# Kernel tuning notes

Measured on AMD Instinct MI355X. Metric: run time of the kernel, lower is better.

## Reference

```python
import jax, jax.numpy as jnp
import numpy as np

B, N, H = 8, 512, 256
D2 = H // 2          # per-direction hidden = attention proj = 128
VOCAB, EMB = 100, 256
DIN0 = EMB + 3


def _sru_pp_layer(x, pad, Wq, Wk, Wv, Wu, vf, vr, bf, br):
    # x: (L, Bt, din); pad: (L, Bt) bool, True = padded position
    L, Bt, _ = x.shape
    d2 = Wu.shape[1] // 8
    q = x @ Wq                                   # (L,Bt,proj) attention projection
    k = q @ Wk
    v = q @ Wv
    scale = 1.0 / jnp.sqrt(jnp.asarray(q.shape[-1], q.dtype))
    scores = jnp.einsum('lbp,mbp->blm', q, k) * scale
    scores = jnp.where(pad.T[:, None, :], -1e9, scores)
    a = jnp.einsum('blm,mbp->lbp', jax.nn.softmax(scores, axis=-1), v) + q
    U = (a @ Wu).reshape(L, Bt, 2, 4, d2)        # 2 directions x 4 matrices

    def run_dir(Ud, padd, vf_d, vr_d, bf_d, br_d):
        def step(c, inp):
            u, p = inp                            # u: (Bt,4,d2), p: (Bt,)
            f = jax.nn.sigmoid(u[:, 1] + vf_d * c + bf_d)
            r = jax.nn.sigmoid(u[:, 2] + vr_d * c + br_d)
            c_new = f * c + (1.0 - f) * u[:, 0]
            c_new = jnp.where(p[:, None], c, c_new)
            h = jnp.where(p[:, None], 0.0, r * c_new + (1.0 - r) * u[:, 3])
            return c_new, h
        c0 = jnp.zeros((Bt, d2), x.dtype)
        _, hs = jax.lax.scan(step, c0, (Ud, padd))
        return hs

    hf = run_dir(U[:, :, 0], pad, vf[0], vr[0], bf[0], br[0])
    hb = run_dir(U[::-1, :, 1], pad[::-1], vf[1], vr[1], bf[1], br[1])[::-1]
    return jnp.concatenate([hf, hb], axis=-1)     # (L,Bt,2*d2)


def _forward(noisy_seqs, noisy_cords, mask, emb, params):
    Bb, Nn = noisy_seqs.shape
    X = noisy_cords[:, :, 1]                      # CA coordinates (B,N,3)
    m3 = mask[..., None]
    center = (X * m3).sum(1) / m3.sum(1)
    Xc = X - center[:, None] * m3
    C = jnp.einsum('bni,bnj->bij', Xc, Xc)        # (B,3,3) covariance
    _, V = jnp.linalg.eigh(jax.lax.stop_gradient(C))
    ops = jnp.asarray([[i, j, k] for i in (-1, 1) for j in (-1, 1) for k in (-1, 1)], X.dtype)
    F_ops = ops[None, :, None, :] * V[:, None]    # (B,8,3,3) sign-flipped frames
    hX = jnp.einsum('boji,bpj->bopi', F_ops, Xc).reshape(Bb * 8, Nn, 3)
    seq = jnp.where(noisy_seqs < 0, 82, noisy_seqs)
    hS = jnp.broadcast_to(emb[seq][:, None], (Bb, 8, Nn, emb.shape[1])).reshape(Bb * 8, Nn, -1)
    h = jnp.swapaxes(jnp.concatenate([hX, hS], -1), 0, 1)   # (N, B*8, EMB+3)
    pad = jnp.broadcast_to((mask == 0.0)[:, None], (Bb, 8, Nn)).reshape(Bb * 8, Nn).T
    for p in params:
        h = _sru_pp_layer(h, pad, *p)
    return jnp.swapaxes(h, 0, 1).reshape(Bb, 8, Nn, -1).mean(1)


def setup_inputs():
    key = jax.random.key(0)
    ks = [jax.random.fold_in(key, i) for i in range(32)]
    inp = {
        'noisy_seqs': jax.random.randint(ks[0], (B, N), 0, VOCAB, dtype=jnp.int32),
        'noisy_cords': jax.random.normal(ks[1], (B, N, 4, 3), jnp.float32),
        'mask': jnp.ones((B, N), jnp.float32),
        'emb': 0.02 * jax.random.normal(ks[2], (VOCAB, EMB), jnp.float32),
    }
    i = 3
    for l, din in enumerate([DIN0, H]):
        inp[f'Wq{l}'] = jax.random.normal(ks[i], (din, D2), jnp.float32) / np.sqrt(din); i += 1
        inp[f'Wk{l}'] = jax.random.normal(ks[i], (D2, D2), jnp.float32) / np.sqrt(D2); i += 1
        inp[f'Wv{l}'] = jax.random.normal(ks[i], (D2, D2), jnp.float32) / np.sqrt(D2); i += 1
        inp[f'Wu{l}'] = jax.random.normal(ks[i], (D2, 8 * D2), jnp.float32) / np.sqrt(D2); i += 1
        inp[f'vf{l}'] = 0.1 * jax.random.normal(ks[i], (2, D2), jnp.float32); i += 1
        inp[f'vr{l}'] = 0.1 * jax.random.normal(ks[i], (2, D2), jnp.float32); i += 1
        inp[f'bf{l}'] = jnp.zeros((2, D2), jnp.float32)
        inp[f'br{l}'] = jnp.zeros((2, D2), jnp.float32)
    return inp


def reference(noisy_seqs, noisy_cords, mask, emb,
              Wq0, Wk0, Wv0, Wu0, vf0, vr0, bf0, br0,
              Wq1, Wk1, Wv1, Wu1, vf1, vr1, bf1, br1):
    params = [(Wq0, Wk0, Wv0, Wu0, vf0, vr0, bf0, br0),
              (Wq1, Wk1, Wv1, Wu1, vf1, vr1, bf1, br1)]
    return _forward(noisy_seqs, noisy_cords, mask, emb, params)
```

## Files before the change

### kernel.cpp

```cpp
#include <hip/hip_runtime.h>
#include <hip/hip_bf16.h>
#include <math.h>

#define L_    512
#define F_    64
#define M_    (F_*L_)
#define D2_   128
#define H_    256
#define LOG2E_ 1.4426950408889634f

typedef unsigned short u16;
typedef __attribute__((ext_vector_type(8))) short s16x8;
typedef __attribute__((ext_vector_type(4))) float f32x4;

__device__ inline u16 bf_hi(float x) {
  union { float f; unsigned u; } v; v.f = x;
  unsigned r = v.u + 0x7fffu + ((v.u >> 16) & 1u);
  return (u16)(r >> 16);
}
__device__ inline float bf_to_f(u16 h) {
  union { float f; unsigned u; } v; v.u = ((unsigned)h) << 16; return v.f;
}
__device__ inline void split2(float x, u16& h, u16& l) {
  h = bf_hi(x);
  l = bf_hi(x - bf_to_f(h));
}
__device__ inline float exp2_fast(float x) {
#if __has_builtin(__builtin_amdgcn_exp2f)
  return __builtin_amdgcn_exp2f(x);
#else
  return __expf(x * 0.6931471805599453f);
#endif
}
__device__ inline float rcp_fast(float x) {
#if __has_builtin(__builtin_amdgcn_rcpf)
  return __builtin_amdgcn_rcpf(x);
#else
  return 1.f/x;
#endif
}

#define RSPLIT_A 18432
#define RSPLIT_B 26624

__global__ void geom_kernel(const float* __restrict__ cords, const float* __restrict__ mask,
                            float* __restrict__ misc) {
  int b = blockIdx.x;
  int t = threadIdx.x;
  __shared__ float red[4][256];
  float sx=0.f, sy=0.f, sz=0.f, sm=0.f;
  for (int l = t; l < 512; l += 256) {
    float m = mask[b*512 + l];
    const float* X = cords + ((size_t)(b*512 + l)*4 + 1)*3;
    sx += X[0]*m; sy += X[1]*m; sz += X[2]*m; sm += m;
  }
  red[0][t]=sx; red[1][t]=sy; red[2][t]=sz; red[3][t]=sm;
  __syncthreads();
  for (int off=128; off>0; off>>=1) {
    if (t < off) { red[0][t]+=red[0][t+off]; red[1][t]+=red[1][t+off];
                   red[2][t]+=red[2][t+off]; red[3][t]+=red[3][t+off]; }
    __syncthreads();
  }
  float inv = 1.f/red[3][0];
  float cx = red[0][0]*inv, cy = red[1][0]*inv, cz = red[2][0]*inv;
  __syncthreads();
  __shared__ float red6[6][256];
  float c00=0,c01=0,c02=0,c11=0,c12=0,c22=0;
  for (int l = t; l < 512; l += 256) {
    float m = mask[b*512+l];
    const float* X = cords + ((size_t)(b*512+l)*4 + 1)*3;
    float x = X[0]-cx*m, y = X[1]-cy*m, z = X[2]-cz*m;
    c00+=x*x; c01+=x*y; c02+=x*z; c11+=y*y; c12+=y*z; c22+=z*z;
  }
  red6[0][t]=c00; red6[1][t]=c01; red6[2][t]=c02;
  red6[3][t]=c11; red6[4][t]=c12; red6[5][t]=c22;
  __syncthreads();
  for (int off=128; off>0; off>>=1) {
    if (t < off) for (int j=0;j<6;j++) red6[j][t]+=red6[j][t+off];
    __syncthreads();
  }
  if (t == 0) {
    double A[3][3], V[3][3];
    A[0][0]=red6[0][0]; A[0][1]=A[1][0]=red6[1][0]; A[0][2]=A[2][0]=red6[2][0];
    A[1][1]=red6[3][0]; A[1][2]=A[2][1]=red6[4][0]; A[2][2]=red6[5][0];
    for (int j=0;j<3;j++) for (int i=0;i<3;i++) V[j][i] = (i==j)?1.0:0.0;
    for (int sweep=0; sweep<10; ++sweep) {
      for (int p=0;p<2;p++) for (int q=p+1;q<3;q++) {
        double apq = A[p][q];
        if (fabs(apq) < 1e-18) continue;
        double app = A[p][p], aqq = A[q][q];
        double tau = (aqq - app) / (2.0*apq);
        double tt = (tau >= 0.0) ? 1.0/(tau + sqrt(1.0+tau*tau))
                                 : 1.0/(tau - sqrt(1.0+tau*tau));
        double cc = 1.0/sqrt(1.0+tt*tt), ss = tt*cc;
        A[p][p] = app - tt*apq;
        A[q][q] = aqq + tt*apq;
        A[p][q] = A[q][p] = 0.0;
        int r = 3 - p - q;
        double arp = A[r][p], arq = A[r][q];
        A[r][p] = A[p][r] = cc*arp - ss*arq;
        A[r][q] = A[q][r] = ss*arp + cc*arq;
        for (int rr2=0; rr2<3; ++rr2) {
          double vrp = V[rr2][p], vrq = V[rr2][q];
          V[rr2][p] = cc*vrp - ss*vrq;
          V[rr2][q] = ss*vrp + cc*vrq;
        }
      }
    }
    double w[3] = {A[0][0], A[1][1], A[2][2]};
    int idx[3] = {0,1,2};
    for (int i=0;i<2;i++) for (int j=0;j<2-i;j++)
      if (w[idx[j]] > w[idx[j+1]]) { int tmp=idx[j]; idx[j]=idx[j+1]; idx[j+1]=tmp; }
    for (int jj=0;jj<3;jj++) for (int ii=0;ii<3;ii++)
      misc[b*12 + jj*3 + ii] = (float)V[jj][idx[ii]];
    misc[b*12+9]=cx; misc[b*12+10]=cy; misc[b*12+11]=cz;
  }
}

__global__ void build_h0(const int* __restrict__ seqs, const float* __restrict__ cords,
                         const float* __restrict__ mask, const float* __restrict__ emb,
                         const float* __restrict__ misc,
                         u16* __restrict__ h0h, u16* __restrict__ h0l) {
  int t = threadIdx.x;
  int r = blockIdx.x*4 + (t >> 6);
  int lane = t & 63;
  int f = r >> 9, l = r & 511;
  int b = f >> 3, o = f & 7;
  u16* rh = h0h + (size_t)r * 288;
  u16* rl = h0l + (size_t)r * 288;
  if (lane == 0) {
    float m = mask[b*512 + l];
    const float* X = cords + ((size_t)(b*512 + l)*4 + 1)*3;
    const float* mb = misc + b*12;
    float x = X[0]-mb[9]*m, y = X[1]-mb[10]*m, z = X[2]-mb[11]*m;
    #pragma unroll
    for (int i=0;i<3;i++) {
      float sgn = ((o >> (2-i)) & 1) ? 1.f : -1.f;
      float val = sgn * (mb[0+i]*x + mb[3+i]*y + mb[6+i]*z);
      u16 h,lo; split2(val,h,lo); rh[i]=h; rl[i]=lo;
    }
  }
  if (lane < 29) { rh[259+lane] = 0; rl[259+lane] = 0; }
  int s = seqs[b*512 + l];
  if (s < 0) s = 82;
  const float4 e4 = *((const float4*)(emb + (size_t)s*256) + lane);
  float ev[4] = {e4.x, e4.y, e4.z, e4.w};
  #pragma unroll
  for (int i=0;i<4;i++) {
    u16 h,lo; split2(ev[i],h,lo);
    rh[3 + lane*4 + i] = h; rl[3 + lane*4 + i] = lo;
  }
}

__global__ void prep_wqkv_mul(const float* __restrict__ Wq, const float* __restrict__ Wk,
                              const float* __restrict__ Wv,
                              float* __restrict__ wqk, float* __restrict__ wqv) {
  int k = blockIdx.x;
  int y = blockIdx.y;
  int t = threadIdx.x;
  __shared__ float row[128];
  row[t] = Wq[(size_t)k*128 + t];
  __syncthreads();
  const float* W2 = y ? Wv : Wk;
  float acc = 0.f;
  for (int j = 0; j < 128; j++) acc += row[j] * W2[(size_t)j*128 + t];
  (y ? wqv : wqk)[(size_t)k*128 + t] = acc;
}

__global__ void prep_wT3(const float* __restrict__ Wq, const float* __restrict__ wqk,
                         const float* __restrict__ wqv,
                         u16* __restrict__ Th, u16* __restrict__ Tl,
                         int K, int KP) {
  int y = blockIdx.y;
  int n = blockIdx.x;
  const float* W = (y==0) ? Wq : (y==1) ? wqk : wqv;
  int row = y*128 + n;
  for (int k = threadIdx.x; k < KP; k += 128) {
    float x = (k < K) ? W[(size_t)k*128 + n] : 0.f;
    u16 h,l; split2(x,h,l);
    Th[(size_t)row*KP + k] = h; Tl[(size_t)row*KP + k] = l;
  }
}

__global__ void prep_wu(const float* __restrict__ Wu, u16* __restrict__ Th, u16* __restrict__ Tl,
                        const float* __restrict__ bfv, const float* __restrict__ brv,
                        float* __restrict__ nbf, float* __restrict__ nbr) {
  int n = blockIdx.x;
  int dir = blockIdx.y;
  int k = threadIdx.x;
  int d = n >> 2, g = n & 3;
  float x = Wu[(size_t)k*1024 + (dir*4+g)*128 + d];
  if (g == 1 || g == 2) x *= -LOG2E_;
  u16 h,l; split2(x,h,l);
  size_t o = ((size_t)dir*512 + n)*128 + k;
  Th[o]=h; Tl[o]=l;
  if (n == 0) {
    nbf[dir*128 + k] = bfv[dir*128 + k] * (-LOG2E_);
    nbr[dir*128 + k] = brv[dir*128 + k] * (-LOG2E_);
  }
}

template<int EPI>
__global__ __launch_bounds__(256) void gemm_bb(
    const u16* __restrict__ Ah, const u16* __restrict__ Al,
    const u16* __restrict__ Bh, const u16* __restrict__ Bl,
    int KP, int lda, int ldb,
    long aBatch, long bBatch, long cBatch,
    u16* __restrict__ Ch, u16* __restrict__ Cl, int ldc,
    u16* __restrict__ Dh, u16* __restrict__ Dl,
    u16* __restrict__ Eh, u16* __restrict__ El,
    float* __restrict__ F0, float* __restrict__ F1, float* __restrict__ F2,
    float* __restrict__ F3, float* __restrict__ F4, float* __restrict__ F5,
    const u16* __restrict__ rh, const u16* __restrict__ rl,
    const float* __restrict__ maskp, const float* __restrict__ nbf,
    const float* __restrict__ nbr, float scale, int dirOff)
{
  __shared__ u16 As[2][128][40];
  __shared__ u16 Bs[2][128][40];
  __shared__ float epsM[128];
  __shared__ float epsA[128];
  const int t = threadIdx.x;
  const int z = blockIdx.z;
  const int bm = blockIdx.x * 128, bn = blockIdx.y * 128;
  Ah += (size_t)z * aBatch; Al += (size_t)z * aBatch;
  Bh += (size_t)z * bBatch; Bl += (size_t)z * bBatch;

  const int lane = t & 63;
  const int w = t >> 6, wr = w >> 1, wc = w & 1;
  const int fr = lane & 15, g = lane >> 4;

  const bool isD1 = (bn >= 512);
  const int dirU = dirOff + (isD1 ? 1 : 0);
  if (EPI == 4) {
    if (t < 128) {
      int r = bm + t;
      epsM[t] = maskp[(r >> 12)*512 + (r & 511)];
      int nl = (bn + t) & 511;
      int dd = nl >> 2, gg2 = nl & 3;
      epsA[t] = (gg2==1) ? nbf[dirU*128 + dd] : (gg2==2) ? nbr[dirU*128 + dd] : 0.f;
    }
  }

  f32x4 acc[4][4] = {};

  for (int k0 = 0; k0 < KP; k0 += 32) {
    #pragma unroll
    for (int cc = 0; cc < 2; cc++) {
      int c = t + cc*256;
      int m = c >> 2, sub = c & 3;
      const size_t ga = (size_t)(bm + m)*lda + k0 + sub*8;
      const size_t gb = (size_t)(bn + m)*ldb + k0 + sub*8;
      *(int4*)&As[0][m][sub*8] = *(const int4*)(Ah + ga);
      *(int4*)&As[1][m][sub*8] = *(const int4*)(Al + ga);
      *(int4*)&Bs[0][m][sub*8] = *(const int4*)(Bh + gb);
      *(int4*)&Bs[1][m][sub*8] = *(const int4*)(Bl + gb);
    }
    __syncthreads();
    s16x8 af[4][2], bfr[4][2];
    #pragma unroll
    for (int i = 0; i < 4; i++) {
      af[i][0]  = *(const s16x8*)&As[0][wr*64 + i*16 + fr][g*8];
      af[i][1]  = *(const s16x8*)&As[1][wr*64 + i*16 + fr][g*8];
      bfr[i][0] = *(const s16x8*)&Bs[0][wc*64 + i*16 + fr][g*8];
      bfr[i][1] = *(const s16x8*)&Bs[1][wc*64 + i*16 + fr][g*8];
    }
    #pragma unroll
    for (int mi = 0; mi < 4; mi++)
      #pragma unroll
      for (int nj = 0; nj < 4; nj++)
        acc[mi][nj] = __builtin_amdgcn_mfma_f32_16x16x32_bf16(af[mi][0], bfr[nj][0], acc[mi][nj], 0,0,0);
    #pragma unroll
    for (int mi = 0; mi < 4; mi++)
      #pragma unroll
      for (int nj = 0; nj < 4; nj++)
        acc[mi][nj] = __builtin_amdgcn_mfma_f32_16x16x32_bf16(af[mi][0], bfr[nj][1], acc[mi][nj], 0,0,0);
    #pragma unroll
    for (int mi = 0; mi < 4; mi++)
      #pragma unroll
      for (int nj = 0; nj < 4; nj++)
        acc[mi][nj] = __builtin_amdgcn_mfma_f32_16x16x32_bf16(af[mi][1], bfr[nj][0], acc[mi][nj], 0,0,0);
    __syncthreads();
  }

  const int rbase = bm + wr*64, nbase = bn + wc*64;
  float* tA = isD1 ? F3 : F0;
  float* tB = isD1 ? F4 : F1;
  float* tC = isD1 ? F5 : F2;
  const int gg = fr & 3;
  const float ovr = (gg==1) ? -16384.f : (gg==2) ? 16384.f : 0.f;

  #pragma unroll
  for (int mi = 0; mi < 4; mi++) {
    #pragma unroll
    for (int nj = 0; nj < 4; nj++) {
      #pragma unroll
      for (int rg = 0; rg < 4; rg++) {
        int r = rbase + mi*16 + g*4 + rg;
        int n = nbase + nj*16 + fr;
        float val = acc[mi][nj][rg];
        if (EPI == 2) {
          float vv = val * scale;
          if (maskp[(z>>3)*512 + n] == 0.f) vv = -1e9f;
          F0[(size_t)z*cBatch + (size_t)r*ldc + n] = vv;
        } else if (EPI == 3) {
          size_t o = (size_t)z*cBatch + (size_t)r*ldc + n;
          float vv = val + (bf_to_f(rh[o]) + bf_to_f(rl[o]));
          u16 h,l; split2(vv,h,l);
          Ch[o]=h; Cl[o]=l;
        } else if (EPI == 4) {
          int nloc = (n & 511);
          val += epsA[n - bn];
          if (epsM[r - bm] == 0.f) val = ovr;
          float* Up;
          if (r < RSPLIT_A)      Up = tA + (size_t)r*512;
          else if (r < RSPLIT_B) Up = tB + (size_t)(r - RSPLIT_A)*512;
          else                   Up = tC + (size_t)(r - RSPLIT_B)*512;
          Up[nloc] = val;
        } else {
          u16 h,l; split2(val,h,l);
          if (blockIdx.y == 0) {
            size_t o = (size_t)r*128 + n;
            Ch[o]=h; Cl[o]=l;
          } else if (blockIdx.y == 1) {
            size_t o = (size_t)r*128 + (n - 128);
            Dh[o]=h; Dl[o]=l;
          } else {
            size_t o = ((size_t)(r >> 9)*128 + (n - 256))*512 + (r & 511);
            Eh[o]=h; El[o]=l;
          }
        }
      }
    }
  }
}

__global__ void softmax_split(float* __restrict__ S) {
  size_t row = blockIdx.x;
  float* p = S + row*512;
  u16* ph = (u16*)p;
  u16* pl = ph + 512;
  int t = threadIdx.x;
  float v[8];
  float mx = -1e30f;
  #pragma unroll
  for (int i=0;i<8;i++) { v[i] = p[t + i*64]; mx = fmaxf(mx, v[i]); }
  #pragma unroll
  for (int off=32; off>0; off>>=1) mx = fmaxf(mx, __shfl_xor(mx, off));
  float sum = 0.f;
  #pragma unroll
  for (int i=0;i<8;i++) { v[i] = __expf(v[i]-mx); sum += v[i]; }
  #pragma unroll
  for (int off=32; off>0; off>>=1) sum += __shfl_xor(sum, off);
  float invs = 1.f/sum;
  #pragma unroll
  for (int i=0;i<8;i++) {
    float x = v[i]*invs;
    u16 h,l; split2(x,h,l);
    ph[t + i*64] = h; pl[t + i*64] = l;
  }
}

#define CH_ 8
#define LOADC(buf, ch) do { \
  int _c = (ch); \
  _Pragma("unroll") \
  for (int s = 0; s < CH_; s++) { \
    int l = (_c*CH_ + s) ^ lxor; \
    buf[s] = *(const float4*)(Ubase + (size_t)l*512); \
  } \
  __builtin_amdgcn_sched_barrier(0); \
} while(0)

#define COMPC(buf, ch) do { \
  int _c = (ch); \
  _Pragma("unroll") \
  for (int s = 0; s < CH_; s++) { \
    int l = (_c*CH_ + s) ^ lxor; \
    float4 u = buf[s]; \
    float ef = exp2_fast(fmaf(nvfd, cstate, u.y)); \
    float fg = rcp_fast(1.f + ef); \
    float er = exp2_fast(fmaf(nvrd, cstate, u.z)); \
    float rg = rcp_fast(1.f + er); \
    float cn = fmaf(fg, cstate - u.x, u.x); \
    float h  = fmaf(rg, cn - u.w, u.w); \
    cstate = cn; \
    if (PAIRS) { \
      u16 sh_, sl_; split2(h, sh_, sl_); \
      hpph[(size_t)l*256] = sh_; \
      hppl[(size_t)l*256] = sl_; \
    } else { \
      h32p[(size_t)l*256] = h; \
    } \
  } \
  __builtin_amdgcn_sched_barrier(0); \
} while(0)

template<int PAIRS>
__global__ __launch_bounds__(64, 1) void sru_scan(
                          const float* __restrict__ ua0, const float* __restrict__ ub0,
                          const float* __restrict__ uc0,
                          const float* __restrict__ ua1, const float* __restrict__ ub1,
                          const float* __restrict__ uc1,
                          const float* __restrict__ vf, const float* __restrict__ vr,
                          u16* __restrict__ hph, u16* __restrict__ hpl,
                          float* __restrict__ h32, int dirArg) {
  const int blk = blockIdx.x;
  const int f = blk >> 1;
  const int hh = blk & 1;
  const int dir = dirArg + blockIdx.y;
  const int t = threadIdx.x;
  const int lxor = dir ? 511 : 0;
  const int d = hh*64 + t;
  const float nvfd = vf[dir*128 + d] * (-LOG2E_);
  const float nvrd = vr[dir*128 + d] * (-LOG2E_);
  const size_t fbase = (size_t)f * 512;
  const float* ua = dir ? ua1 : ua0;
  const float* ub = dir ? ub1 : ub0;
  const float* uc = dir ? uc1 : uc0;
  const float* Uf;
  if (f < 36)      Uf = ua + (size_t)f*(512*512);
  else if (f < 52) Uf = ub + (size_t)(f-36)*(512*512);
  else             Uf = uc + (size_t)(f-52)*(512*512);
  const float* Ubase = Uf + d*4;
  u16* hpph = hph + fbase*256 + (size_t)dir*128 + d;
  u16* hppl = hpl + fbase*256 + (size_t)dir*128 + d;
  float* h32p = h32 + fbase*256 + (size_t)dir*128 + d;

  float4 b0[CH_], b1[CH_], b2[CH_], b3[CH_];
  LOADC(b0, 0); LOADC(b1, 1);
  float cstate = 0.f;
  #pragma unroll 1
  for (int q4 = 0; q4 < 15; q4++) {
    const int base = q4*4;
    LOADC(b2, base+2);
    COMPC(b0, base);
    LOADC(b3, base+3);
    COMPC(b1, base+1);
    LOADC(b0, base+4);
    COMPC(b2, base+2);
    LOADC(b1, base+5);
    COMPC(b3, base+3);
  }
  LOADC(b2, 62);
  COMPC(b0, 60);
  LOADC(b3, 63);
  COMPC(b1, 61);
  COMPC(b2, 62);
  COMPC(b3, 63);
}

__global__ void mean_kernel(const float* __restrict__ h2, float* __restrict__ out) {
  int i = blockIdx.x*256 + threadIdx.x;
  int row = i >> 6;
  int c4  = i & 63;
  int b = row >> 9, l = row & 511;
  float ax=0.f, ay=0.f, az=0.f, aw=0.f;
  #pragma unroll
  for (int o=0;o<8;o++) {
    const float4* p = (const float4*)(h2 + ((size_t)((b*8+o)*512 + l))*256) + c4;
    float4 e = *p;
    ax += e.x; ay += e.y; az += e.z; aw += e.w;
  }
  float4 r; r.x = ax*0.125f; r.y = ay*0.125f; r.z = az*0.125f; r.w = aw*0.125f;
  ((float4*)out)[i] = r;
}

extern "C" void kernel_launch(void* const* d_in, const int* in_sizes, int n_in,
                              void* d_out, int out_size, void* d_ws, size_t ws_size,
                              hipStream_t stream) {
  const int*   seqs  = (const int*)d_in[0];
  const float* cords = (const float*)d_in[1];
  const float* mask  = (const float*)d_in[2];
  const float* emb   = (const float*)d_in[3];
  const float* Wq[2] = {(const float*)d_in[4],  (const float*)d_in[12]};
  const float* Wk[2] = {(const float*)d_in[5],  (const float*)d_in[13]};
  const float* Wv[2] = {(const float*)d_in[6],  (const float*)d_in[14]};
  const float* Wu[2] = {(const float*)d_in[7],  (const float*)d_in[15]};
  const float* vf[2] = {(const float*)d_in[8],  (const float*)d_in[16]};
  const float* vr[2] = {(const float*)d_in[9],  (const float*)d_in[17]};
  const float* bfp[2]= {(const float*)d_in[10], (const float*)d_in[18]};
  const float* brp[2]= {(const float*)d_in[11], (const float*)d_in[19]};

  const size_t H0_B = 2*(size_t)M_*288*2;
  const size_t Q_B  = 2*(size_t)M_*128*2;
  const size_t S_B  = (size_t)M_*512*4;
  const size_t HP_B = 2*(size_t)M_*256*2;
  const size_t W_B  = (size_t)(2*1024*128)*2 + 2*256*4;

  const size_t NEED_MERGED = 4096 + H0_B + 3*Q_B + S_B + HP_B + W_B;
  const bool merged = (ws_size >= NEED_MERGED);

  char* base = (char*)d_ws;
  float* misc = (float*)base;
  u16* h0p_h = (u16*)(base + 4096);
  u16* h0p_l = h0p_h + (size_t)M_*288;
  u16* q_h   = (u16*)(base + 4096 + H0_B);
  u16* q_l   = q_h + (size_t)M_*128;
  u16* k_h   = (u16*)(base + 4096 + H0_B + Q_B);
  u16* k_l   = k_h + (size_t)M_*128;
  u16* a_h = k_h;  u16* a_l = k_l;

  u16 *vT_h, *vT_l;
  float *S, *tail_w;
  u16 *hp_h, *hp_l;
  float *U1A, *U1B, *U1C;
  if (merged) {
    vT_h = (u16*)(base + 4096 + H0_B + 2*Q_B);
    vT_l = vT_h + (size_t)M_*128;
    S    = (float*)(base + 4096 + H0_B + 3*Q_B);
    hp_h = (u16*)((char*)S + S_B);
    hp_l = hp_h + (size_t)M_*256;
    tail_w = (float*)((char*)hp_h + HP_B);
    U1A = (float*)h0p_h;
    U1B = (float*)q_h;
    U1C = (float*)vT_h;
  } else {
    S    = (float*)(base + 4096 + H0_B + 2*Q_B);
    hp_h = (u16*)((char*)S + S_B);
    hp_l = hp_h + (size_t)M_*256;
    vT_h = hp_h; vT_l = hp_l;
    tail_w = (float*)((char*)hp_h + HP_B);
    U1A = S; U1B = S + (size_t)RSPLIT_A*512; U1C = S + (size_t)RSPLIT_B*512;
  }
  float* U0A = S;
  float* U0B = S + (size_t)RSPLIT_A*512;
  float* U0C = S + (size_t)RSPLIT_B*512;
  float* h32 = (float*)hp_h;

  float* wqk32 = S;
  float* wqv32 = wqk32 + 288*128;
  u16*   wT3h  = (u16*)(wqv32 + 288*128);
  u16*   wT3l  = wT3h + 384*288;
  u16* wuT_h = (u16*)tail_w;
  u16* wuT_l = wuT_h + 1024*128;
  float* nbf = (float*)(wuT_l + 1024*128);
  float* nbr = nbf + 256;

  geom_kernel<<<8, 256, 0, stream>>>(cords, mask, misc);
  build_h0<<<M_/4, 256, 0, stream>>>(seqs, cords, mask, emb, misc, h0p_h, h0p_l);

  const float scale = 0.08838834764831845f;
  for (int layer = 0; layer < 2; ++layer) {
    const u16* Ah_in = layer ? hp_h : h0p_h;
    const u16* Al_in = layer ? hp_l : h0p_l;
    const int  Kq    = layer ? 256 : 259;
    const int  KPq   = layer ? 256 : 288;

    prep_wqkv_mul<<<dim3(Kq,2), 128, 0, stream>>>(Wq[layer], Wk[layer], Wv[layer], wqk32, wqv32);
    prep_wT3<<<dim3(128,3), 128, 0, stream>>>(Wq[layer], wqk32, wqv32, wT3h, wT3l, Kq, KPq);
    prep_wu<<<dim3(512,2), 128, 0, stream>>>(Wu[layer], wuT_h, wuT_l, bfp[layer], brp[layer], nbf, nbr);

    gemm_bb<5><<<dim3(256,3,1), 256, 0, stream>>>(Ah_in, Al_in, wT3h, wT3l,
        KPq, KPq, KPq, 0,0,0, q_h, q_l, 128, k_h, k_l, vT_h, vT_l,
        nullptr,nullptr,nullptr,nullptr,nullptr,nullptr,
        nullptr,nullptr, nullptr,nullptr,nullptr, 0.f, 0);
    gemm_bb<2><<<dim3(4,4,64), 256, 0, stream>>>(q_h, q_l, k_h, k_l,
        128, 128, 128, 512*128, 512*128, 512*512, nullptr,nullptr, 512,
        nullptr,nullptr,nullptr,nullptr,
        S,nullptr,nullptr,nullptr,nullptr,nullptr,
        nullptr,nullptr, mask,nullptr,nullptr, scale, 0);
    softmax_split<<<M_, 64, 0, stream>>>(S);
    gemm_bb<3><<<dim3(4,1,64), 256, 0, stream>>>((const u16*)S, (const u16*)S + 512, vT_h, vT_l,
        512, 1024, 512, 512*1024, 128*512, 512*128, a_h, a_l, 128,
        nullptr,nullptr,nullptr,nullptr,
        nullptr,nullptr,nullptr,nullptr,nullptr,nullptr,
        q_h, q_l, nullptr,nullptr,nullptr, 0.f, 0);

    if (merged) {
      gemm_bb<4><<<dim3(256,8,1), 256, 0, stream>>>(a_h, a_l, wuT_h, wuT_l,
          128, 128, 128, 0,0,0, nullptr,nullptr, 512,
          nullptr,nullptr,nullptr,nullptr,
          U0A,U0B,U0C, U1A,U1B,U1C,
          nullptr,nullptr, mask, nbf, nbr, 0.f, 0);
      if (layer == 0)
        sru_scan<1><<<dim3(128,2), 64, 0, stream>>>(U0A,U0B,U0C, U1A,U1B,U1C,
            vf[layer], vr[layer], hp_h, hp_l, h32, 0);
      else
        sru_scan<0><<<dim3(128,2), 64, 0, stream>>>(U0A,U0B,U0C, U1A,U1B,U1C,
            vf[layer], vr[layer], hp_h, hp_l, h32, 0);
    } else {
      for (int dir = 0; dir < 2; ++dir) {
        gemm_bb<4><<<dim3(256,4,1), 256, 0, stream>>>(a_h, a_l,
            wuT_h + (size_t)dir*512*128, wuT_l + (size_t)dir*512*128,
            128, 128, 128, 0,0,0, nullptr,nullptr, 512,
            nullptr,nullptr,nullptr,nullptr,
            U0A,U0B,U0C, U0A,U0B,U0C,
            nullptr,nullptr, mask, nbf, nbr, 0.f, dir);
        if (layer == 0)
          sru_scan<1><<<dim3(128,1), 64, 0, stream>>>(U0A,U0B,U0C, U0A,U0B,U0C,
              vf[layer], vr[layer], hp_h, hp_l, h32, dir);
        else
          sru_scan<0><<<dim3(128,1), 64, 0, stream>>>(U0A,U0B,U0C, U0A,U0B,U0C,
              vf[layer], vr[layer], hp_h, hp_l, h32, dir);
      }
    }
  }
  mean_kernel<<<1024, 256, 0, stream>>>(h32, (float*)d_out);
}
```

Before: 495.9 us.

## Fuse QK^T, masked softmax and PV into a flash-attention kernel

Result: faster. 468.4 us (-5.5%).

```diff
diff --git a/kernel.cpp b/kernel.cpp
--- a/kernel.cpp
+++ b/kernel.cpp
@@ -334,6 +334,219 @@
   }
 }
 
+__global__ __launch_bounds__(256) void attn_flash(
+    const u16* __restrict__ qh, const u16* __restrict__ ql,
+    const u16* __restrict__ kh, const u16* __restrict__ kl,
+    const u16* __restrict__ vTh, const u16* __restrict__ vTl,
+    const float* __restrict__ maskp,
+    u16* __restrict__ ah, u16* __restrict__ al, float scale)
+{
+  __shared__ u16 As[2][64][36];
+  __shared__ u16 Bs[2][128][36];
+  __shared__ u16 Ps[2][64][68];
+  __shared__ float rmaxL[2][64];
+  __shared__ float rsumL[2][64];
+  __shared__ float mskt[64];
+  const int t = threadIdx.x;
+  const int f = blockIdx.y;
+  const int bq = f >> 3;
+  const int bm = blockIdx.x * 64;
+  const size_t qrow0 = (size_t)f*512 + bm;
+  const int lane = t & 63;
+  const int w = t >> 6, wr = w >> 1, wc = w & 1;
+  const int fr = lane & 15, g = lane >> 4;
+  const int m_ = t >> 2, sub_ = t & 3;
+
+  float mrun[2][4], srun[2][4];
+  #pragma unroll
+  for (int mi=0;mi<2;mi++)
+    #pragma unroll
+    for (int rg=0;rg<4;rg++) { mrun[mi][rg] = -3e38f; srun[mi][rg] = 0.f; }
+  f32x4 Oacc[2][4] = {};
+
+  for (int kt = 0; kt < 8; ++kt) {
+    if (t < 64) mskt[t] = maskp[bq*512 + kt*64 + t];
+    f32x4 Sacc[2][2] = {};
+    #pragma unroll
+    for (int k0 = 0; k0 < 4; ++k0) {
+      {
+        const size_t ga = (qrow0 + m_)*128 + k0*32 + sub_*8;
+        const size_t gb = ((size_t)f*512 + kt*64 + m_)*128 + k0*32 + sub_*8;
+        *(int4*)&As[0][m_][sub_*8] = *(const int4*)(qh + ga);
+        *(int4*)&As[1][m_][sub_*8] = *(const int4*)(ql + ga);
+        *(int4*)&Bs[0][m_][sub_*8] = *(const int4*)(kh + gb);
+        *(int4*)&Bs[1][m_][sub_*8] = *(const int4*)(kl + gb);
+      }
+      __syncthreads();
+      s16x8 af[2][2], bf2[2][2];
+      #pragma unroll
+      for (int i = 0; i < 2; i++) {
+        af[i][0]  = *(const s16x8*)&As[0][wr*32 + i*16 + fr][g*8];
+        af[i][1]  = *(const s16x8*)&As[1][wr*32 + i*16 + fr][g*8];
+        bf2[i][0] = *(const s16x8*)&Bs[0][wc*32 + i*16 + fr][g*8];
+        bf2[i][1] = *(const s16x8*)&Bs[1][wc*32 + i*16 + fr][g*8];
+      }
+      #pragma unroll
+      for (int mi = 0; mi < 2; mi++)
+        #pragma unroll
+        for (int nj = 0; nj < 2; nj++)
+          Sacc[mi][nj] = __builtin_amdgcn_mfma_f32_16x16x32_bf16(af[mi][0], bf2[nj][0], Sacc[mi][nj], 0,0,0);
+      #pragma unroll
+      for (int mi = 0; mi < 2; mi++)
+        #pragma unroll
+        for (int nj = 0; nj < 2; nj++)
+          Sacc[mi][nj] = __builtin_amdgcn_mfma_f32_16x16x32_bf16(af[mi][0], bf2[nj][1], Sacc[mi][nj], 0,0,0);
+      #pragma unroll
+      for (int mi = 0; mi < 2; mi++)
+        #pragma unroll
+        for (int nj = 0; nj < 2; nj++)
+          Sacc[mi][nj] = __builtin_amdgcn_mfma_f32_16x16x32_bf16(af[mi][1], bf2[nj][0], Sacc[mi][nj], 0,0,0);
+      __syncthreads();
+    }
+    float mkv[2];
+    mkv[0] = mskt[wc*32 + fr];
+    mkv[1] = mskt[wc*32 + 16 + fr];
+    float rm[2][4];
+    #pragma unroll
+    for (int mi=0;mi<2;mi++)
+      #pragma unroll
+      for (int rg=0;rg<4;rg++) rm[mi][rg] = -3e38f;
+    #pragma unroll
+    for (int mi=0;mi<2;mi++)
+      #pragma unroll
+      for (int nj=0;nj<2;nj++)
+        #pragma unroll
+        for (int rg=0;rg<4;rg++) {
+          float sv = Sacc[mi][nj][rg]*scale;
+          sv = (mkv[nj]==0.f) ? -1e9f : sv;
+          Sacc[mi][nj][rg] = sv;
+          rm[mi][rg] = fmaxf(rm[mi][rg], sv);
+        }
+    #pragma unroll
+    for (int off=1; off<16; off<<=1)
+      #pragma unroll
+      for (int mi=0;mi<2;mi++)
+        #pragma unroll
+        for (int rg=0;rg<4;rg++) rm[mi][rg] = fmaxf(rm[mi][rg], __shfl_xor(rm[mi][rg], off));
+    if (fr == 0) {
+      #pragma unroll
+      for (int mi=0;mi<2;mi++)
+        #pragma unroll
+        for (int rg=0;rg<4;rg++) rmaxL[wc][wr*32 + mi*16 + g*4 + rg] = rm[mi][rg];
+    }
+    __syncthreads();
+    float alpha[2][4], rs[2][4];
+    #pragma unroll
+    for (int mi=0;mi<2;mi++)
+      #pragma unroll
+      for (int rg=0;rg<4;rg++) {
+        int rl_ = wr*32 + mi*16 + g*4 + rg;
+        float tmax = fmaxf(rmaxL[0][rl_], rmaxL[1][rl_]);
+        float mn = fmaxf(mrun[mi][rg], tmax);
+        alpha[mi][rg] = exp2_fast((mrun[mi][rg] - mn)*LOG2E_);
+        mrun[mi][rg] = mn;
+        rs[mi][rg] = 0.f;
+      }
+    #pragma unroll
+    for (int mi=0;mi<2;mi++)
+      #pragma unroll
+      for (int nj=0;nj<2;nj++)
+        #pragma unroll
+        for (int rg=0;rg<4;rg++) {
+          float p = exp2_fast((Sacc[mi][nj][rg] - mrun[mi][rg])*LOG2E_);
+          rs[mi][rg] += p;
+          u16 h,l; split2(p,h,l);
+          int rl_ = wr*32 + mi*16 + g*4 + rg;
+          int cl_ = wc*32 + nj*16 + fr;
+          Ps[0][rl_][cl_] = h;
+          Ps[1][rl_][cl_] = l;
+        }
+    #pragma unroll
+    for (int off=1; off<16; off<<=1)
+      #pragma unroll
+      for (int mi=0;mi<2;mi++)
+        #pragma unroll
+        for (int rg=0;rg<4;rg++) rs[mi][rg] += __shfl_xor(rs[mi][rg], off);
+    if (fr == 0) {
+      #pragma unroll
+      for (int mi=0;mi<2;mi++)
+        #pragma unroll
+        for (int rg=0;rg<4;rg++) rsumL[wc][wr*32 + mi*16 + g*4 + rg] = rs[mi][rg];
+    }
+    #pragma unroll
+    for (int mi=0;mi<2;mi++)
+      #pragma unroll
+      for (int nj=0;nj<4;nj++)
+        #pragma unroll
+        for (int rg=0;rg<4;rg++) Oacc[mi][nj][rg] *= alpha[mi][rg];
+    __syncthreads();
+    #pragma unroll
+    for (int mi=0;mi<2;mi++)
+      #pragma unroll
+      for (int rg=0;rg<4;rg++) {
+        int rl_ = wr*32 + mi*16 + g*4 + rg;
+        srun[mi][rg] = srun[mi][rg]*alpha[mi][rg] + rsumL[0][rl_] + rsumL[1][rl_];
+      }
+    #pragma unroll
+    for (int k0 = 0; k0 < 2; ++k0) {
+      #pragma unroll
+      for (int cc = 0; cc < 2; cc++) {
+        int c = t + cc*256;
+        int mv = c >> 2, sb = c & 3;
+        const size_t gv = ((size_t)f*128 + mv)*512 + kt*64 + k0*32 + sb*8;
+        *(int4*)&Bs[0][mv][sb*8] = *(const int4*)(vTh + gv);
+        *(int4*)&Bs[1][mv][sb*8] = *(const int4*)(vTl + gv);
+      }
+      __syncthreads();
+      s16x8 pa[2][2], pb[4][2];
+      #pragma unroll
+      for (int i = 0; i < 2; i++) {
+        pa[i][0] = *(const s16x8*)&Ps[0][wr*32 + i*16 + fr][k0*32 + g*8];
+        pa[i][1] = *(const s16x8*)&Ps[1][wr*32 + i*16 + fr][k0*32 + g*8];
+      }
+      #pragma unroll
+      for (int j = 0; j < 4; j++) {
+        pb[j][0] = *(const s16x8*)&Bs[0][wc*64 + j*16 + fr][g*8];
+        pb[j][1] = *(const s16x8*)&Bs[1][wc*64 + j*16 + fr][g*8];
+      }
+      #pragma unroll
+      for (int mi = 0; mi < 2; mi++)
+        #pragma unroll
+        for (int nj = 0; nj < 4; nj++)
+          Oacc[mi][nj] = __builtin_amdgcn_mfma_f32_16x16x32_bf16(pa[mi][0], pb[nj][0], Oacc[mi][nj], 0,0,0);
+      #pragma unroll
+      for (int mi = 0; mi < 2; mi++)
+        #pragma unroll
+        for (int nj = 0; nj < 4; nj++)
+          Oacc[mi][nj] = __builtin_amdgcn_mfma_f32_16x16x32_bf16(pa[mi][0], pb[nj][1], Oacc[mi][nj], 0,0,0);
+      #pragma unroll
+      for (int mi = 0; mi < 2; mi++)
+        #pragma unroll
+        for (int nj = 0; nj < 4; nj++)
+          Oacc[mi][nj] = __builtin_amdgcn_mfma_f32_16x16x32_bf16(pa[mi][1], pb[nj][0], Oacc[mi][nj], 0,0,0);
+      __syncthreads();
+    }
+  }
+  float inv[2][4];
+  #pragma unroll
+  for (int mi=0;mi<2;mi++)
+    #pragma unroll
+    for (int rg=0;rg<4;rg++) inv[mi][rg] = 1.f / srun[mi][rg];
+  #pragma unroll
+  for (int mi=0;mi<2;mi++)
+    #pragma unroll
+    for (int nj=0;nj<4;nj++)
+      #pragma unroll
+      for (int rg=0;rg<4;rg++) {
+        int rl_ = wr*32 + mi*16 + g*4 + rg;
+        int cl_ = wc*64 + nj*16 + fr;
+        size_t o = (qrow0 + rl_)*128 + cl_;
+        float val = Oacc[mi][nj][rg]*inv[mi][rg] + bf_to_f(qh[o]) + bf_to_f(ql[o]);
+        u16 h,l; split2(val,h,l);
+        ah[o]=h; al[o]=l;
+      }
+}
+
 __global__ void softmax_split(float* __restrict__ S) {
   size_t row = blockIdx.x;
   float* p = S + row*512;
@@ -498,9 +711,8 @@
   u16* q_l   = q_h + (size_t)M_*128;
   u16* k_h   = (u16*)(base + 4096 + H0_B + Q_B);
   u16* k_l   = k_h + (size_t)M_*128;
-  u16* a_h = k_h;  u16* a_l = k_l;
-
-  u16 *vT_h, *vT_l;
+
+  u16 *vT_h, *vT_l, *a_h, *a_l;
   float *S, *tail_w;
   u16 *hp_h, *hp_l;
   float *U1A, *U1B, *U1C;
@@ -514,6 +726,8 @@
     U1A = (float*)h0p_h;
     U1B = (float*)q_h;
     U1C = (float*)vT_h;
+    a_h = hp_h;
+    a_l = hp_h + (size_t)M_*128;
   } else {
     S    = (float*)(base + 4096 + H0_B + 2*Q_B);
     hp_h = (u16*)((char*)S + S_B);
@@ -521,6 +735,7 @@
     vT_h = hp_h; vT_l = hp_l;
     tail_w = (float*)((char*)hp_h + HP_B);
     U1A = S; U1B = S + (size_t)RSPLIT_A*512; U1C = S + (size_t)RSPLIT_B*512;
+    a_h = k_h; a_l = k_l;
   }
   float* U0A = S;
   float* U0B = S + (size_t)RSPLIT_A*512;
@@ -554,17 +769,23 @@
         KPq, KPq, KPq, 0,0,0, q_h, q_l, 128, k_h, k_l, vT_h, vT_l,
         nullptr,nullptr,nullptr,nullptr,nullptr,nullptr,
         nullptr,nullptr, nullptr,nullptr,nullptr, 0.f, 0);
-    gemm_bb<2><<<dim3(4,4,64), 256, 0, stream>>>(q_h, q_l, k_h, k_l,
-        128, 128, 128, 512*128, 512*128, 512*512, nullptr,nullptr, 512,
-        nullptr,nullptr,nullptr,nullptr,
-        S,nullptr,nullptr,nullptr,nullptr,nullptr,
-        nullptr,nullptr, mask,nullptr,nullptr, scale, 0);
-    softmax_split<<<M_, 64, 0, stream>>>(S);
-    gemm_bb<3><<<dim3(4,1,64), 256, 0, stream>>>((const u16*)S, (const u16*)S + 512, vT_h, vT_l,
-        512, 1024, 512, 512*1024, 128*512, 512*128, a_h, a_l, 128,
-        nullptr,nullptr,nullptr,nullptr,
-        nullptr,nullptr,nullptr,nullptr,nullptr,nullptr,
-        q_h, q_l, nullptr,nullptr,nullptr, 0.f, 0);
+
+    if (merged) {
+      attn_flash<<<dim3(8,64), 256, 0, stream>>>(q_h, q_l, k_h, k_l, vT_h, vT_l,
+          mask, a_h, a_l, scale);
+    } else {
+      gemm_bb<2><<<dim3(4,4,64), 256, 0, stream>>>(q_h, q_l, k_h, k_l,
+          128, 128, 128, 512*128, 512*128, 512*512, nullptr,nullptr, 512,
+          nullptr,nullptr,nullptr,nullptr,
+          S,nullptr,nullptr,nullptr,nullptr,nullptr,
+          nullptr,nullptr, mask,nullptr,nullptr, scale, 0);
+      softmax_split<<<M_, 64, 0, stream>>>(S);
+      gemm_bb<3><<<dim3(4,1,64), 256, 0, stream>>>((const u16*)S, (const u16*)S + 512, vT_h, vT_l,
+          512, 1024, 512, 512*1024, 128*512, 512*128, a_h, a_l, 128,
+          nullptr,nullptr,nullptr,nullptr,
+          nullptr,nullptr,nullptr,nullptr,nullptr,nullptr,
+          q_h, q_l, nullptr,nullptr,nullptr, 0.f, 0);
+    }
 
     if (merged) {
       gemm_bb<4><<<dim3(256,8,1), 256, 0, stream>>>(a_h, a_l, wuT_h, wuT_l,
```
